# Kernel optimization log

Hardware: AMD Instinct MI355X
Metric: run time of the kernel (lower is better)

The kernel has to match this reference:

```python
import jax, jax.numpy as jnp
import numpy as np
from jax.scipy.special import logsumexp

REG_E = 0.05
N_ITER = 20


def setup_inputs() -> dict:
    key = jax.random.key(0)
    kP, kQ = jax.random.split(key)
    n, m, d = 8192, 8192, 64
    XP = jax.random.normal(kP, (n, d), dtype=jnp.float32)
    XQ = jax.random.normal(kQ, (m, d), dtype=jnp.float32)
    return {"XP": XP, "XQ": XQ}


def sq_cdist(X, Y):
    # squared euclidean distances, (n, m)
    x2 = jnp.sum(X * X, axis=1, keepdims=True)          # (n,1)
    y2 = jnp.sum(Y * Y, axis=1, keepdims=True).T        # (1,m)
    d2 = x2 + y2 - 2.0 * (X @ Y.T)
    return jnp.maximum(d2, 0.0)


def log_sinkhorn(log_a, log_b, C, reg, n_iter):
    # stable log-domain Sinkhorn; returns transport plan exp(M + u[:,None] + v[None,:])
    M = -C / reg                                        # (n,m)
    u0 = jnp.zeros_like(log_a)
    v0 = jnp.zeros_like(log_b)

    def body(carry, _):
        u, v = carry
        u = log_a - logsumexp(M + v[None, :], axis=1)
        v = log_b - logsumexp(M + u[:, None], axis=0)
        return (u, v), None

    (u, v), _ = jax.lax.scan(body, (u0, v0), None, length=n_iter)
    return jnp.exp(M + u[:, None] + v[None, :])


def reference(XP, XQ):
    n, m = XP.shape[0], XQ.shape[0]
    log_uP = jnp.full((n,), -jnp.log(jnp.float32(n)), dtype=XP.dtype)
    log_uQ = jnp.full((m,), -jnp.log(jnp.float32(m)), dtype=XQ.dtype)

    C = sq_cdist(XP, XQ)                                # (n, m)
    Cn = C / jax.lax.stop_gradient(jnp.max(C))
    plan = jax.lax.stop_gradient(
        log_sinkhorn(log_uP, log_uQ, Cn, REG_E, N_ITER)
    )
    return jnp.sum(C * plan)
```

## Files before the change

### kernel.cpp

```cpp
#include <hip/hip_runtime.h>
#include <cmath>

#define NPTS 8192
#define DIM  64
#define LOG2E 1.4426950408889634f
#define LA2   -13.0f
#define NSWEEP 40

typedef short s16x8  __attribute__((ext_vector_type(8)));
typedef float f32x16 __attribute__((ext_vector_type(16)));

typedef __attribute__((address_space(1))) const unsigned char g8_t;
typedef __attribute__((address_space(3))) unsigned char l8_t;

#if __has_builtin(__builtin_amdgcn_exp2f)
__device__ __forceinline__ float exp2_fast(float x) { return __builtin_amdgcn_exp2f(x); }
#else
__device__ __forceinline__ float exp2_fast(float x) { return exp2f(x); }
#endif
#if __has_builtin(__builtin_amdgcn_logf)
__device__ __forceinline__ float log2_fast(float x) { return __builtin_amdgcn_logf(x); }
#else
__device__ __forceinline__ float log2_fast(float x) { return log2f(x); }
#endif

__device__ __forceinline__ unsigned short f2bf(float x) {
  unsigned u = __float_as_uint(x);
  return (unsigned short)((u + 0x7FFFu + ((u >> 16) & 1u)) >> 16);
}
__device__ __forceinline__ float bf2f(unsigned short b) {
  return __uint_as_float(((unsigned)b) << 16);
}

__global__ __launch_bounds__(256) void prep_kernel(
    const float* __restrict__ XP, const float* __restrict__ XQ,
    unsigned short* __restrict__ Phi, unsigned short* __restrict__ Plo,
    unsigned short* __restrict__ Qhi, unsigned short* __restrict__ Qlo,
    float* __restrict__ x2, float* __restrict__ y2,
    float* __restrict__ partS,
    float* __restrict__ scal, float* __restrict__ out) {
  int gid  = blockIdx.x * 256 + threadIdx.x;
  int lane = threadIdx.x & 63;
  int row  = gid >> 6;
  int isP  = row < NPTS;
  int r    = row & (NPTS - 1);
  const float* X = isP ? XP : XQ;
  float x = X[r * DIM + lane];
  unsigned short h = f2bf(x);
  (isP ? Phi : Qhi)[r * DIM + lane] = h;
  (isP ? Plo : Qlo)[r * DIM + lane] = f2bf(x - bf2f(h));
  float s = x * x;
  for (int off = 32; off; off >>= 1) s += __shfl_down(s, off, 64);
  if (lane == 0) (isP ? x2 : y2)[r] = s;
  if (gid < NSWEEP * NPTS) partS[gid] = 0.0f;
  if (gid == 0) { ((unsigned*)scal)[0] = 0u; out[0] = 0.0f; }
}

template <int MODE, bool FIRST, int MINW>
__global__ __launch_bounds__(256, MINW) void pass_kernel(
    const unsigned short* __restrict__ Ahi, const unsigned short* __restrict__ Alo,
    const unsigned short* __restrict__ Bhi,
    const float* __restrict__ x2row, const float* __restrict__ y2col,
    const float* __restrict__ colPart,
    const float* __restrict__ rowPart,
    const unsigned* __restrict__ cmaxBits,
    float* __restrict__ outPart, float* __restrict__ outScalar) {
  __shared__ short sB[2][128 * DIM];
  __shared__ float sCol[512];
  __shared__ float sY2[512];
  __shared__ float sX2[128];
  __shared__ float sU2[128];
  __shared__ float sRed[4];

  const int t  = threadIdx.x;
  const int w  = t >> 6;
  const int l  = t & 63;
  const int g  = l >> 5;
  const int ln = l & 31;
  const int i0 = blockIdx.x * 128;
  const int j0 = blockIdx.y * 512;

  float invC = 0.f, C2L = 0.f;
  if constexpr (MODE != 0) {
    float cmax = __uint_as_float(*cmaxBits);
    invC = 1.0f / (0.05f * cmax);
    C2L  = 2.0f * invC * LOG2E;
  }

  const int gOff   = (w * 32 + (l >> 3)) * 128 + (((l & 7) ^ (l >> 3)) * 16);
  const int ldsOff = w * 4096 + l * 16;
  auto stage = [&](int qq, int bi) {
    const unsigned char* src =
        (const unsigned char*)(Bhi + (size_t)(j0 + qq * 128) * DIM) + gOff;
    unsigned char* dst = (unsigned char*)(&sB[bi][0]) + ldsOff;
#pragma unroll
    for (int c = 0; c < 4; ++c)
      __builtin_amdgcn_global_load_lds((g8_t*)(src + c * 1024),
                                       (l8_t*)(dst + c * 1024), 16, 0, 0);
  };

  stage(0, 0);
  stage(1, 1);

  s16x8 a_hi[4], a_lo[4];
  {
    const unsigned short* pa = Ahi + (size_t)(i0 + w * 32 + ln) * DIM + g * 8;
#pragma unroll
    for (int ks = 0; ks < 4; ++ks) a_hi[ks] = *(const s16x8*)(pa + ks * 16);
    if constexpr (MODE == 2) {
      const unsigned short* pb = Alo + (size_t)(i0 + w * 32 + ln) * DIM + g * 8;
#pragma unroll
      for (int ks = 0; ks < 4; ++ks) a_lo[ks] = *(const s16x8*)(pb + ks * 16);
    }
  }

#pragma unroll
  for (int c0 = 0; c0 < 2; ++c0) {
    int c = c0 * 256 + t;
    int j = j0 + c;
    if constexpr (MODE == 0) {
      sY2[c] = y2col[j];
    } else if constexpr (MODE == 1) {
      if constexpr (FIRST) {
        sCol[c] = -invC * y2col[j] * LOG2E;
      } else {
        sCol[c] = LA2 - log2_fast(colPart[j]);
      }
    } else {
      sCol[c] = LA2 - log2_fast(colPart[j]);
      sY2[c] = y2col[j];
    }
  }
  if constexpr (MODE != 1) {
    if (t < 128) {
      sX2[t] = x2row[i0 + t];
      if constexpr (MODE == 2)
        sU2[t] = LA2 - log2_fast(rowPart[i0 + t]);
    }
  }
  __syncthreads();

  float x2r[16], u2r[16];
  if constexpr (MODE != 1) {
#pragma unroll
    for (int r = 0; r < 16; ++r) {
      int ri = w * 32 + (r & 3) + 8 * (r >> 2) + 4 * g;
      x2r[r] = sX2[ri];
      if constexpr (MODE == 2) u2r[r] = sU2[ri];
    }
  }

  float racc[16];
#pragma unroll
  for (int r = 0; r < 16; ++r) racc[r] = 0.f;
  float accS = 0.f;

  auto do_quarter = [&](const short* __restrict__ buf, int qq) {
#pragma unroll 2
    for (int ct = 0; ct < 4; ++ct) {
      const int nn = ct * 32 + ln;
      const int n  = qq * 128 + ct * 32 + ln;
      s16x8 b[4];
#pragma unroll
      for (int ks = 0; ks < 4; ++ks)
        b[ks] = *(const s16x8*)(buf + nn * DIM + (((ks * 2 + g) ^ (ln & 7)) * 8));
      f32x16 acc;
#pragma unroll
      for (int r = 0; r < 16; ++r) acc[r] = 0.f;
#pragma unroll
      for (int ks = 0; ks < 4; ++ks)
        acc = __builtin_amdgcn_mfma_f32_32x32x16_bf16(a_hi[ks], b[ks], acc, 0, 0, 0);

      if constexpr (MODE == 1) {
        const float bb = sCol[n];
#pragma unroll
        for (int r = 0; r < 16; ++r)
          racc[r] += exp2_fast(fmaf(C2L, acc[r], bb));
      } else if constexpr (MODE == 0) {
        const float y2v = sY2[n];
#pragma unroll
        for (int r = 0; r < 16; ++r)
          accS = fmaxf(accS, fmaf(-2.0f, acc[r], x2r[r] + y2v));
      } else {
        f32x16 acc2;
#pragma unroll
        for (int r = 0; r < 16; ++r) acc2[r] = 0.f;
#pragma unroll
        for (int ks = 0; ks < 4; ++ks)
          acc2 = __builtin_amdgcn_mfma_f32_32x32x16_bf16(a_lo[ks], b[ks], acc2, 0, 0, 0);
        const float y2v = sY2[n];
        const float bb  = sCol[n];
#pragma unroll
        for (int r = 0; r < 16; ++r) {
          float dot = acc[r] + acc2[r];
          float d2  = fmaxf(fmaf(-2.0f, dot, x2r[r] + y2v), 0.0f);
          accS = fmaf(d2, exp2_fast(fmaf(C2L, dot, u2r[r] + bb)), accS);
        }
      }
    }
  };

  do_quarter(sB[0], 0);
  __syncthreads();
  stage(2, 0);
  do_quarter(sB[1], 1);
  __syncthreads();
  stage(3, 1);
  do_quarter(sB[0], 2);
  __syncthreads();
  do_quarter(sB[1], 3);

  if constexpr (MODE == 1) {
#pragma unroll
    for (int r = 0; r < 16; ++r) {
      float v = racc[r];
      v += __shfl_xor(v, 1, 64);
      v += __shfl_xor(v, 2, 64);
      v += __shfl_xor(v, 4, 64);
      v += __shfl_xor(v, 8, 64);
      v += __shfl_xor(v, 16, 64);
      if (ln == 0)
        atomicAdd(&outPart[i0 + w * 32 + (r & 3) + 8 * (r >> 2) + 4 * g], v);
    }
  } else {
    float v = accS;
#pragma unroll
    for (int off = 1; off < 64; off <<= 1) {
      float o = __shfl_xor(v, off, 64);
      v = (MODE == 0) ? fmaxf(v, o) : (v + o);
    }
    if (l == 0) sRed[w] = v;
    __syncthreads();
    if (t == 0) {
      float r0 = (MODE == 0) ? fmaxf(fmaxf(sRed[0], sRed[1]), fmaxf(sRed[2], sRed[3]))
                             : (sRed[0] + sRed[1] + sRed[2] + sRed[3]);
      if constexpr (MODE == 0)
        atomicMax((unsigned*)outScalar, __float_as_uint(r0));
      else
        atomicAdd(outScalar, r0);
    }
  }
}

extern "C" void kernel_launch(void* const* d_in, const int* in_sizes, int n_in,
                              void* d_out, int out_size, void* d_ws, size_t ws_size,
                              hipStream_t stream) {
  (void)in_sizes; (void)n_in; (void)out_size; (void)ws_size;
  const float* XP = (const float*)d_in[0];
  const float* XQ = (const float*)d_in[1];
  float* out = (float*)d_out;

  float* ws    = (float*)d_ws;
  float* x2    = ws;
  float* y2    = ws + 8192;
  float* partS = ws + 16384;
  float* scal  = partS + NSWEEP * NPTS;
  unsigned short* Phi = (unsigned short*)(scal + 16);
  unsigned short* Plo = Phi + (size_t)NPTS * DIM;
  unsigned short* Qhi = Plo + (size_t)NPTS * DIM;
  unsigned short* Qlo = Qhi + (size_t)NPTS * DIM;

  const unsigned* cmaxB = (const unsigned*)scal;
  dim3 grid(NPTS / 128, NPTS / 512);

  prep_kernel<<<NPTS * 2 * DIM / 256, 256, 0, stream>>>(
      XP, XQ, Phi, Plo, Qhi, Qlo, x2, y2, partS, scal, out);

  pass_kernel<0, false, 4><<<grid, 256, 0, stream>>>(
      Phi, nullptr, Qhi, x2, y2, nullptr, nullptr, cmaxB, nullptr, scal);

  auto reg = [&](int s) { return partS + (size_t)s * NPTS; };

  pass_kernel<1, true, 4><<<grid, 256, 0, stream>>>(
      Phi, nullptr, Qhi, nullptr, y2, nullptr, nullptr, cmaxB, reg(0), nullptr);
  pass_kernel<1, false, 4><<<grid, 256, 0, stream>>>(
      Qhi, nullptr, Phi, nullptr, nullptr, reg(0), nullptr, cmaxB, reg(1), nullptr);

  for (int it = 1; it < 20; ++it) {
    int s = it * 2;
    pass_kernel<1, false, 4><<<grid, 256, 0, stream>>>(
        Phi, nullptr, Qhi, nullptr, nullptr, reg(s - 1), nullptr, cmaxB, reg(s), nullptr);
    pass_kernel<1, false, 4><<<grid, 256, 0, stream>>>(
        Qhi, nullptr, Phi, nullptr, nullptr, reg(s), nullptr, cmaxB, reg(s + 1), nullptr);
  }

  pass_kernel<2, false, 2><<<grid, 256, 0, stream>>>(
      Phi, Plo, Qhi, x2, y2, reg(39), reg(38), cmaxB, nullptr, out);
}
```

Baseline: 820.5 us.

## Add dedicated sweep kernel with per-wave double-buffered async LDS staging

Splits the Sinkhorn sweep (MODE 1) out of the generic pass kernel into a dedicated kernel. Each wave stages its own 32-column chunks of B into a private double buffer using global_load_lds and synchronises with explicit vmcnt/lgkmcnt waits instead of block-wide barriers. The aim is to overlap global loads with MFMA and exp work and to remove __syncthreads stalls in the 40 sweep launches. In exchange, each wave loads the whole B tile on its own (4x redundant global traffic per block), and correctness relies on hand-placed waitcnt ordering.

New measurement: 918.9 us. +12.0%, slower.

```diff
diff --git a/kernel.cpp b/kernel.cpp
--- a/kernel.cpp
+++ b/kernel.cpp
@@ -56,7 +56,103 @@
   if (gid == 0) { ((unsigned*)scal)[0] = 0u; out[0] = 0.0f; }
 }
 
-template <int MODE, bool FIRST, int MINW>
+template <bool FIRST>
+__global__ __launch_bounds__(256, 4) void sweep_kernel(
+    const unsigned short* __restrict__ Ahi,
+    const unsigned short* __restrict__ Bhi,
+    const float* __restrict__ y2col,
+    const float* __restrict__ colPart,
+    const unsigned* __restrict__ cmaxBits,
+    float* __restrict__ outPart) {
+  __shared__ short sB[4][2][32 * DIM];
+  __shared__ float sCol[512];
+
+  const int t  = threadIdx.x;
+  const int w  = t >> 6;
+  const int l  = t & 63;
+  const int g  = l >> 5;
+  const int ln = l & 31;
+  const int i0 = blockIdx.x * 128;
+  const int j0 = blockIdx.y * 512;
+
+  const float cmax = __uint_as_float(*cmaxBits);
+  const float invC = 1.0f / (0.05f * cmax);
+  const float C2L  = 2.0f * invC * LOG2E;
+
+  const int gOffW = (l >> 3) * 128 + (((l & 7) ^ (l >> 3)) * 16);
+  auto stage = [&](int chunk, int bi) {
+    const unsigned char* src =
+        (const unsigned char*)(Bhi + (size_t)(j0 + chunk * 32) * DIM) + gOffW;
+    unsigned char* dst = (unsigned char*)(&sB[w][bi][0]) + l * 16;
+#pragma unroll
+    for (int cc2 = 0; cc2 < 4; ++cc2)
+      __builtin_amdgcn_global_load_lds((g8_t*)(src + cc2 * 1024),
+                                       (l8_t*)(dst + cc2 * 1024), 16, 0, 0);
+  };
+
+  stage(0, 0);
+  stage(1, 1);
+
+  s16x8 a_hi[4];
+  {
+    const unsigned short* pa = Ahi + (size_t)(i0 + w * 32 + ln) * DIM + g * 8;
+#pragma unroll
+    for (int ks = 0; ks < 4; ++ks) a_hi[ks] = *(const s16x8*)(pa + ks * 16);
+  }
+
+#pragma unroll
+  for (int c0 = 0; c0 < 2; ++c0) {
+    int c = c0 * 256 + t;
+    int j = j0 + c;
+    if constexpr (FIRST) {
+      sCol[c] = -invC * y2col[j] * LOG2E;
+    } else {
+      sCol[c] = LA2 - log2_fast(colPart[j]);
+    }
+  }
+  __syncthreads();
+
+  float racc[16];
+#pragma unroll
+  for (int r = 0; r < 16; ++r) racc[r] = 0.f;
+
+#pragma unroll 2
+  for (int c = 0; c < 16; ++c) {
+    const int bi = c & 1;
+    asm volatile("s_waitcnt vmcnt(4)" ::: "memory");
+    const short* buf = &sB[w][bi][0];
+    s16x8 b[4];
+#pragma unroll
+    for (int ks = 0; ks < 4; ++ks)
+      b[ks] = *(const s16x8*)(buf + ln * DIM + (((ks * 2 + g) ^ (ln & 7)) * 8));
+    const float bb = sCol[c * 32 + ln];
+    f32x16 acc;
+#pragma unroll
+    for (int r = 0; r < 16; ++r) acc[r] = 0.f;
+#pragma unroll
+    for (int ks = 0; ks < 4; ++ks)
+      acc = __builtin_amdgcn_mfma_f32_32x32x16_bf16(a_hi[ks], b[ks], acc, 0, 0, 0);
+    asm volatile("s_waitcnt lgkmcnt(0)" ::: "memory");
+    if (c + 2 < 16) stage(c + 2, bi);
+#pragma unroll
+    for (int r = 0; r < 16; ++r)
+      racc[r] += exp2_fast(fmaf(C2L, acc[r], bb));
+  }
+
+#pragma unroll
+  for (int r = 0; r < 16; ++r) {
+    float v = racc[r];
+    v += __shfl_xor(v, 1, 64);
+    v += __shfl_xor(v, 2, 64);
+    v += __shfl_xor(v, 4, 64);
+    v += __shfl_xor(v, 8, 64);
+    v += __shfl_xor(v, 16, 64);
+    if (ln == 0)
+      atomicAdd(&outPart[i0 + w * 32 + (r & 3) + 8 * (r >> 2) + 4 * g], v);
+  }
+}
+
+template <int MODE, int MINW>
 __global__ __launch_bounds__(256, MINW) void pass_kernel(
     const unsigned short* __restrict__ Ahi, const unsigned short* __restrict__ Alo,
     const unsigned short* __restrict__ Bhi,
@@ -64,7 +160,7 @@
     const float* __restrict__ colPart,
     const float* __restrict__ rowPart,
     const unsigned* __restrict__ cmaxBits,
-    float* __restrict__ outPart, float* __restrict__ outScalar) {
+    float* __restrict__ outScalar) {
   __shared__ short sB[2][128 * DIM];
   __shared__ float sCol[512];
   __shared__ float sY2[512];
@@ -120,39 +216,26 @@
     int j = j0 + c;
     if constexpr (MODE == 0) {
       sY2[c] = y2col[j];
-    } else if constexpr (MODE == 1) {
-      if constexpr (FIRST) {
-        sCol[c] = -invC * y2col[j] * LOG2E;
-      } else {
-        sCol[c] = LA2 - log2_fast(colPart[j]);
-      }
     } else {
       sCol[c] = LA2 - log2_fast(colPart[j]);
       sY2[c] = y2col[j];
     }
   }
-  if constexpr (MODE != 1) {
-    if (t < 128) {
-      sX2[t] = x2row[i0 + t];
-      if constexpr (MODE == 2)
-        sU2[t] = LA2 - log2_fast(rowPart[i0 + t]);
-    }
+  if (t < 128) {
+    sX2[t] = x2row[i0 + t];
+    if constexpr (MODE == 2)
+      sU2[t] = LA2 - log2_fast(rowPart[i0 + t]);
   }
   __syncthreads();
 
   float x2r[16], u2r[16];
-  if constexpr (MODE != 1) {
-#pragma unroll
-    for (int r = 0; r < 16; ++r) {
-      int ri = w * 32 + (r & 3) + 8 * (r >> 2) + 4 * g;
-      x2r[r] = sX2[ri];
-      if constexpr (MODE == 2) u2r[r] = sU2[ri];
-    }
-  }
-
-  float racc[16];
-#pragma unroll
-  for (int r = 0; r < 16; ++r) racc[r] = 0.f;
+#pragma unroll
+  for (int r = 0; r < 16; ++r) {
+    int ri = w * 32 + (r & 3) + 8 * (r >> 2) + 4 * g;
+    x2r[r] = sX2[ri];
+    if constexpr (MODE == 2) u2r[r] = sU2[ri];
+  }
+
   float accS = 0.f;
 
   auto do_quarter = [&](const short* __restrict__ buf, int qq) {
@@ -171,12 +254,7 @@
       for (int ks = 0; ks < 4; ++ks)
         acc = __builtin_amdgcn_mfma_f32_32x32x16_bf16(a_hi[ks], b[ks], acc, 0, 0, 0);
 
-      if constexpr (MODE == 1) {
-        const float bb = sCol[n];
-#pragma unroll
-        for (int r = 0; r < 16; ++r)
-          racc[r] += exp2_fast(fmaf(C2L, acc[r], bb));
-      } else if constexpr (MODE == 0) {
+      if constexpr (MODE == 0) {
         const float y2v = sY2[n];
 #pragma unroll
         for (int r = 0; r < 16; ++r)
@@ -210,35 +288,21 @@
   __syncthreads();
   do_quarter(sB[1], 3);
 
-  if constexpr (MODE == 1) {
-#pragma unroll
-    for (int r = 0; r < 16; ++r) {
-      float v = racc[r];
-      v += __shfl_xor(v, 1, 64);
-      v += __shfl_xor(v, 2, 64);
-      v += __shfl_xor(v, 4, 64);
-      v += __shfl_xor(v, 8, 64);
-      v += __shfl_xor(v, 16, 64);
-      if (ln == 0)
-        atomicAdd(&outPart[i0 + w * 32 + (r & 3) + 8 * (r >> 2) + 4 * g], v);
-    }
-  } else {
-    float v = accS;
-#pragma unroll
-    for (int off = 1; off < 64; off <<= 1) {
-      float o = __shfl_xor(v, off, 64);
-      v = (MODE == 0) ? fmaxf(v, o) : (v + o);
-    }
-    if (l == 0) sRed[w] = v;
-    __syncthreads();
-    if (t == 0) {
-      float r0 = (MODE == 0) ? fmaxf(fmaxf(sRed[0], sRed[1]), fmaxf(sRed[2], sRed[3]))
-                             : (sRed[0] + sRed[1] + sRed[2] + sRed[3]);
-      if constexpr (MODE == 0)
-        atomicMax((unsigned*)outScalar, __float_as_uint(r0));
-      else
-        atomicAdd(outScalar, r0);
-    }
+  float v = accS;
+#pragma unroll
+  for (int off = 1; off < 64; off <<= 1) {
+    float o = __shfl_xor(v, off, 64);
+    v = (MODE == 0) ? fmaxf(v, o) : (v + o);
+  }
+  if (l == 0) sRed[w] = v;
+  __syncthreads();
+  if (t == 0) {
+    float r0 = (MODE == 0) ? fmaxf(fmaxf(sRed[0], sRed[1]), fmaxf(sRed[2], sRed[3]))
+                           : (sRed[0] + sRed[1] + sRed[2] + sRed[3]);
+    if constexpr (MODE == 0)
+      atomicMax((unsigned*)outScalar, __float_as_uint(r0));
+    else
+      atomicAdd(outScalar, r0);
   }
 }
 
@@ -266,24 +330,24 @@
   prep_kernel<<<NPTS * 2 * DIM / 256, 256, 0, stream>>>(
       XP, XQ, Phi, Plo, Qhi, Qlo, x2, y2, partS, scal, out);
 
-  pass_kernel<0, false, 4><<<grid, 256, 0, stream>>>(
-      Phi, nullptr, Qhi, x2, y2, nullptr, nullptr, cmaxB, nullptr, scal);
+  pass_kernel<0, 4><<<grid, 256, 0, stream>>>(
+      Phi, nullptr, Qhi, x2, y2, nullptr, nullptr, cmaxB, scal);
 
   auto reg = [&](int s) { return partS + (size_t)s * NPTS; };
 
-  pass_kernel<1, true, 4><<<grid, 256, 0, stream>>>(
-      Phi, nullptr, Qhi, nullptr, y2, nullptr, nullptr, cmaxB, reg(0), nullptr);
-  pass_kernel<1, false, 4><<<grid, 256, 0, stream>>>(
-      Qhi, nullptr, Phi, nullptr, nullptr, reg(0), nullptr, cmaxB, reg(1), nullptr);
+  sweep_kernel<true><<<grid, 256, 0, stream>>>(
+      Phi, Qhi, y2, nullptr, cmaxB, reg(0));
+  sweep_kernel<false><<<grid, 256, 0, stream>>>(
+      Qhi, Phi, nullptr, reg(0), cmaxB, reg(1));
 
   for (int it = 1; it < 20; ++it) {
     int s = it * 2;
-    pass_kernel<1, false, 4><<<grid, 256, 0, stream>>>(
-        Phi, nullptr, Qhi, nullptr, nullptr, reg(s - 1), nullptr, cmaxB, reg(s), nullptr);
-    pass_kernel<1, false, 4><<<grid, 256, 0, stream>>>(
-        Qhi, nullptr, Phi, nullptr, nullptr, reg(s), nullptr, cmaxB, reg(s + 1), nullptr);
-  }
-
-  pass_kernel<2, false, 2><<<grid, 256, 0, stream>>>(
-      Phi, Plo, Qhi, x2, y2, reg(39), reg(38), cmaxB, nullptr, out);
-}
+    sweep_kernel<false><<<grid, 256, 0, stream>>>(
+        Phi, Qhi, nullptr, reg(s - 1), cmaxB, reg(s));
+    sweep_kernel<false><<<grid, 256, 0, stream>>>(
+        Qhi, Phi, nullptr, reg(s), cmaxB, reg(s + 1));
+  }
+
+  pass_kernel<2, 2><<<grid, 256, 0, stream>>>(
+      Phi, Plo, Qhi, x2, y2, reg(39), reg(38), cmaxB, out);
+}
```
